# Kernel tuning notes

Measured on AMD Instinct MI355X. Metric: run time of the kernel, lower is better.

The kernel has to match this reference:

```python
import jax, jax.numpy as jnp
import numpy as np

D_MODEL = 1024
NHEAD = 16
DFF = 4096
EPS = 1e-5


def layer_norm(x, g, b, eps=EPS):
    mu = jnp.mean(x, axis=-1, keepdims=True)
    var = jnp.var(x, axis=-1, keepdims=True)
    return (x - mu) * jax.lax.rsqrt(var + eps) * g + b


def setup_inputs() -> dict:
    key = jax.random.key(0)
    ks = jax.random.split(key, 8)
    S, N, E = 1024, 8, D_MODEL
    s = 0.02
    return {
        "src": jax.random.normal(ks[0], (S, N, E), dtype=jnp.float32),
        "in_proj_w": jax.random.normal(ks[1], (3 * E, E), dtype=jnp.float32) * s,
        "in_proj_b": jnp.zeros((3 * E,), dtype=jnp.float32),
        "out_w": jax.random.normal(ks[2], (E, E), dtype=jnp.float32) * s,
        "out_b": jnp.zeros((E,), dtype=jnp.float32),
        "w1": jax.random.normal(ks[3], (DFF, E), dtype=jnp.float32) * s,
        "b1": jnp.zeros((DFF,), dtype=jnp.float32),
        "w2": jax.random.normal(ks[4], (E, DFF), dtype=jnp.float32) * s,
        "b2": jnp.zeros((E,), dtype=jnp.float32),
        "ln1_g": jnp.ones((E,), dtype=jnp.float32),
        "ln1_b": jnp.zeros((E,), dtype=jnp.float32),
        "ln2_g": jnp.ones((E,), dtype=jnp.float32),
        "ln2_b": jnp.zeros((E,), dtype=jnp.float32),
    }


def reference(src, in_proj_w, in_proj_b, out_w, out_b, w1, b1, w2, b2,
              ln1_g, ln1_b, ln2_g, ln2_b):
    S, N, E = src.shape
    H = NHEAD
    D = E // H
    scale = 1.0 / jnp.sqrt(jnp.asarray(D, src.dtype))

    # fused QKV projection (PyTorch in_proj): [S,N,3E]
    qkv = src @ in_proj_w.T + in_proj_b
    q, k, v = jnp.split(qkv, 3, axis=-1)
    # [S,N,E] -> [N,H,S,D]
    def to_heads(t):
        return t.reshape(S, N, H, D).transpose(1, 2, 0, 3)
    q, k, v = to_heads(q), to_heads(k), to_heads(v)

    # explicit QK^T / softmax / AV (need_weights=True path)
    scores = jnp.einsum('nhsd,nhtd->nhst', q * scale, k)  # [N,H,S,S]
    attn = jax.nn.softmax(scores, axis=-1)
    ctx = jnp.einsum('nhst,nhtd->nhsd', attn, v)          # [N,H,S,D]
    ctx = ctx.transpose(2, 0, 1, 3).reshape(S, N, E)
    attn_out = ctx @ out_w.T + out_b

    # avg over heads (PyTorch default average_attn_weights=True): [N,S,S]
    attn_weights = jnp.mean(attn, axis=1)

    # post-norm residual structure (norm_first=False), dropout=0 (eval)
    x = layer_norm(src + attn_out, ln1_g, ln1_b)
    ff = jax.nn.relu(x @ w1.T + b1) @ w2.T + b2
    x = layer_norm(x + ff, ln2_g, ln2_b)
    return x, attn_weights
```

## Files before the change

### kernel.cpp

```cpp
#include <hip/hip_runtime.h>

typedef __attribute__((ext_vector_type(4))) float f32x4;
typedef __attribute__((ext_vector_type(8))) short short8;
typedef __attribute__((ext_vector_type(4))) unsigned short u16x4;

#define MFMA(a,b,c) __builtin_amdgcn_mfma_f32_16x16x32_bf16(a,b,c,0,0,0)

__device__ __forceinline__ unsigned short f2bf(float x){
    union { float f; unsigned int u; } c; c.f = x;
    unsigned int u = c.u;
    unsigned int r = (u + 0x7fffu + ((u >> 16) & 1u)) >> 16;
    return (unsigned short)r;
}
__device__ __forceinline__ float bf2f(unsigned short h){
    union { unsigned int u; float f; } c; c.u = ((unsigned int)h) << 16;
    return c.f;
}

__device__ __forceinline__ void load16_lds(const unsigned short* g, unsigned short* l){
    __builtin_amdgcn_global_load_lds(
        (const __attribute__((address_space(1))) unsigned int*)g,
        (__attribute__((address_space(3))) unsigned int*)l, 16, 0, 0);
}

#define SWZ_IDX(row, col, stride) \
    ((row)*(stride) + (((((col) >> 3) ^ ((row) & 7)) << 3) | ((col) & 7)))

__global__ __launch_bounds__(256) void cast_f32_bf16(const float* __restrict__ in,
                                                     unsigned short* __restrict__ out, int n4){
    int i = blockIdx.x * 256 + threadIdx.x;
    if (i < n4){
        const float4* in4 = (const float4*)in;
        float4 v = in4[i];
        u16x4 o;
        o[0] = f2bf(v.x); o[1] = f2bf(v.y); o[2] = f2bf(v.z); o[3] = f2bf(v.w);
        ((u16x4*)out)[i] = o;
    }
}

template<int OUT_BF16, int RELU>
__global__ __launch_bounds__(512) void gemm256(const unsigned short* __restrict__ A,
                                               const unsigned short* __restrict__ W,
                                               const float* __restrict__ bias,
                                               void* __restrict__ Cout,
                                               int M, int N, int K)
{
    __shared__ unsigned short Asw[2][256*64];
    __shared__ unsigned short Bsw[2][256*64];
    const int tid  = threadIdx.x;
    const int wave = tid >> 6, lane = tid & 63;
    const int wr = wave >> 2, wc = wave & 3;
    const int lr = lane & 15, lg = lane >> 4;
    const int bm = blockIdx.x, bn = blockIdx.y;

    f32x4 acc[8][4] = {};

    const unsigned short* Ab = A + (size_t)bm*256*K;
    const unsigned short* Wb = W + (size_t)bn*256*K;

    auto stage = [&](int buf, int k0){
        #pragma unroll
        for (int i = 0; i < 4; ++i){
            int c = i*512 + tid;
            int row = c >> 3, sl = (c & 7) ^ (row & 7);
            load16_lds(Ab + (size_t)row*K + k0 + sl*8, &Asw[buf][0] + (size_t)c*8);
        }
        #pragma unroll
        for (int i = 0; i < 4; ++i){
            int c = i*512 + tid;
            int row = c >> 3, sl = (c & 7) ^ (row & 7);
            load16_lds(Wb + (size_t)row*K + k0 + sl*8, &Bsw[buf][0] + (size_t)c*8);
        }
    };

    stage(0, 0);
    const int NT = K >> 6;
    for (int t = 0; t < NT; ++t){
        const int cur = t & 1;
        if (t + 1 < NT){
            stage(cur ^ 1, (t+1) << 6);
            asm volatile("s_waitcnt vmcnt(8)" ::: "memory");
        } else {
            asm volatile("s_waitcnt vmcnt(0)" ::: "memory");
        }
        __builtin_amdgcn_s_barrier();
        asm volatile("" ::: "memory");
        const unsigned short* Al = &Asw[cur][0];
        const unsigned short* Bl = &Bsw[cur][0];
        #pragma unroll
        for (int kk = 0; kk < 2; ++kk){
            short8 af[8], bf[4];
            #pragma unroll
            for (int mi = 0; mi < 8; ++mi)
                af[mi] = *(const short8*)(Al + SWZ_IDX(wr*128 + mi*16 + lr, kk*32 + lg*8, 64));
            #pragma unroll
            for (int ni = 0; ni < 4; ++ni)
                bf[ni] = *(const short8*)(Bl + SWZ_IDX(wc*64 + ni*16 + lr, kk*32 + lg*8, 64));
            __builtin_amdgcn_s_setprio(1);
            #pragma unroll
            for (int mi = 0; mi < 8; ++mi)
                #pragma unroll
                for (int ni = 0; ni < 4; ++ni)
                    acc[mi][ni] = MFMA(af[mi], bf[ni], acc[mi][ni]);
            __builtin_amdgcn_s_setprio(0);
        }
        asm volatile("" ::: "memory");
        __builtin_amdgcn_s_barrier();
    }

    #pragma unroll
    for (int ni = 0; ni < 4; ++ni){
        int col = bn*256 + wc*64 + ni*16 + lr;
        float bv = bias ? bias[col] : 0.0f;
        #pragma unroll
        for (int mi = 0; mi < 8; ++mi){
            int row0 = bm*256 + wr*128 + mi*16 + lg*4;
            #pragma unroll
            for (int j = 0; j < 4; ++j){
                float v = acc[mi][ni][j] + bv;
                if (RELU) v = v > 0.0f ? v : 0.0f;
                if (OUT_BF16) ((unsigned short*)Cout)[(size_t)(row0+j)*N + col] = f2bf(v);
                else          ((float*)Cout)[(size_t)(row0+j)*N + col] = v;
            }
        }
    }
}

template<int OUT_BF16, int RELU>
__global__ __launch_bounds__(512) void gemm256x128(const unsigned short* __restrict__ A,
                                                   const unsigned short* __restrict__ W,
                                                   const float* __restrict__ bias,
                                                   void* __restrict__ Cout,
                                                   int M, int N, int K)
{
    __shared__ unsigned short Asw[2][256*64];
    __shared__ unsigned short Bsw[2][128*64];
    const int tid  = threadIdx.x;
    const int wave = tid >> 6, lane = tid & 63;
    const int wr = wave >> 1, wc = wave & 1;
    const int lr = lane & 15, lg = lane >> 4;
    const int bm = blockIdx.x, bn = blockIdx.y;

    f32x4 acc[4][4] = {};

    const unsigned short* Ab = A + (size_t)bm*256*K;
    const unsigned short* Wb = W + (size_t)bn*128*K;

    auto stage = [&](int buf, int k0){
        #pragma unroll
        for (int i = 0; i < 4; ++i){
            int c = i*512 + tid;
            int row = c >> 3, sl = (c & 7) ^ (row & 7);
            load16_lds(Ab + (size_t)row*K + k0 + sl*8, &Asw[buf][0] + (size_t)c*8);
        }
        #pragma unroll
        for (int i = 0; i < 2; ++i){
            int c = i*512 + tid;
            int row = c >> 3, sl = (c & 7) ^ (row & 7);
            load16_lds(Wb + (size_t)row*K + k0 + sl*8, &Bsw[buf][0] + (size_t)c*8);
        }
    };

    stage(0, 0);
    const int NT = K >> 6;
    for (int t = 0; t < NT; ++t){
        const int cur = t & 1;
        if (t + 1 < NT){
            stage(cur ^ 1, (t+1) << 6);
            asm volatile("s_waitcnt vmcnt(6)" ::: "memory");
        } else {
            asm volatile("s_waitcnt vmcnt(0)" ::: "memory");
        }
        __builtin_amdgcn_s_barrier();
        asm volatile("" ::: "memory");
        const unsigned short* Al = &Asw[cur][0];
        const unsigned short* Bl = &Bsw[cur][0];
        #pragma unroll
        for (int kk = 0; kk < 2; ++kk){
            short8 af[4], bf[4];
            #pragma unroll
            for (int mi = 0; mi < 4; ++mi)
                af[mi] = *(const short8*)(Al + SWZ_IDX(wr*64 + mi*16 + lr, kk*32 + lg*8, 64));
            #pragma unroll
            for (int ni = 0; ni < 4; ++ni)
                bf[ni] = *(const short8*)(Bl + SWZ_IDX(wc*64 + ni*16 + lr, kk*32 + lg*8, 64));
            __builtin_amdgcn_s_setprio(1);
            #pragma unroll
            for (int mi = 0; mi < 4; ++mi)
                #pragma unroll
                for (int ni = 0; ni < 4; ++ni)
                    acc[mi][ni] = MFMA(af[mi], bf[ni], acc[mi][ni]);
            __builtin_amdgcn_s_setprio(0);
        }
        asm volatile("" ::: "memory");
        __builtin_amdgcn_s_barrier();
    }

    #pragma unroll
    for (int ni = 0; ni < 4; ++ni){
        int col = bn*128 + wc*64 + ni*16 + lr;
        float bv = bias ? bias[col] : 0.0f;
        #pragma unroll
        for (int mi = 0; mi < 4; ++mi){
            int row0 = bm*256 + wr*64 + mi*16 + lg*4;
            #pragma unroll
            for (int j = 0; j < 4; ++j){
                float v = acc[mi][ni][j] + bv;
                if (RELU) v = v > 0.0f ? v : 0.0f;
                if (OUT_BF16) ((unsigned short*)Cout)[(size_t)(row0+j)*N + col] = f2bf(v);
                else          ((float*)Cout)[(size_t)(row0+j)*N + col] = v;
            }
        }
    }
}

__global__ __launch_bounds__(256) void transpose_v(const unsigned short* __restrict__ qkv,
                                                   unsigned short* __restrict__ vt)
{
    __shared__ unsigned short tile[64][80];
    const int tt = blockIdx.x, h = blockIdx.y, n = blockIdx.z;
    const int tid = threadIdx.x;
    #pragma unroll
    for (int i = 0; i < 2; ++i){
        int c = i*256 + tid;
        int row = c >> 3, cc = c & 7;
        short8 v = *(const short8*)(qkv + ((size_t)(tt*64+row)*8 + n)*3072 + 2048 + h*64 + cc*8);
        *(short8*)&tile[row][cc*8] = v;
    }
    __syncthreads();
    #pragma unroll
    for (int i = 0; i < 2; ++i){
        int c = i*256 + tid;
        int drow = c >> 3, cc = c & 7;
        short8 o;
        #pragma unroll
        for (int j = 0; j < 8; ++j) o[j] = tile[cc*8+j][drow];
        *(short8*)(vt + ((size_t)(n*16+h)*64 + drow)*1024 + tt*64 + cc*8) = o;
    }
}

__global__ __launch_bounds__(256) void attn_fused(const unsigned short* __restrict__ qkv,
                                                  const unsigned short* __restrict__ vt,
                                                  float2* __restrict__ stats,
                                                  unsigned short* __restrict__ ctx)
{
    __shared__ unsigned short qs[32*64];
    __shared__ unsigned short kt[64*64];
    __shared__ unsigned short vtile[64*64];
    __shared__ unsigned short pt[32*64];
    __shared__ float wl[4][32];
    __shared__ float rowinv[32];
    const int qb = blockIdx.x, h = blockIdx.y, n = blockIdx.z;
    const int tid = threadIdx.x;
    const int wave = tid >> 6, lane = tid & 63;
    const int lr = lane & 15, lg = lane >> 4;
    const int s0 = qb * 32;
    const float scale = 0.125f;

    {
        int row = tid >> 3, cc = tid & 7;
        *(short8*)(qs + SWZ_IDX(row, cc*8, 64)) =
            *(const short8*)(qkv + ((size_t)(s0+row)*8 + n)*3072 + h*64 + cc*8);
    }

    float lsum[2][4] = {};
    f32x4 av[2] = {};

    for (int tt = 0; tt < 16; ++tt){
        __syncthreads();
        #pragma unroll
        for (int i = 0; i < 2; ++i){
            int c = i*256 + wave*64 + lane;
            int row = c >> 3, sl = (c & 7) ^ (row & 7);
            load16_lds(qkv + ((size_t)(tt*64+row)*8 + n)*3072 + 1024 + h*64 + sl*8,
                       kt + (size_t)(i*256 + wave*64)*8);
            load16_lds(vt + ((size_t)(n*16+h)*64 + row)*1024 + tt*64 + sl*8,
                       vtile + (size_t)(i*256 + wave*64)*8);
        }
        __syncthreads();

        f32x4 acc[2] = {};
        #pragma unroll
        for (int kk = 0; kk < 2; ++kk){
            short8 b  = *(const short8*)(kt + SWZ_IDX(wave*16 + lr, kk*32 + lg*8, 64));
            short8 a0 = *(const short8*)(qs + SWZ_IDX(lr,          kk*32 + lg*8, 64));
            short8 a1 = *(const short8*)(qs + SWZ_IDX(16 + lr,     kk*32 + lg*8, 64));
            acc[0] = MFMA(a0, b, acc[0]);
            acc[1] = MFMA(a1, b, acc[1]);
        }
        #pragma unroll
        for (int mi = 0; mi < 2; ++mi)
            #pragma unroll
            for (int j = 0; j < 4; ++j){
                float p = __expf(fminf(acc[mi][j] * scale, 80.0f));
                lsum[mi][j] += p;
                pt[SWZ_IDX(mi*16 + lg*4 + j, wave*16 + lr, 64)] = f2bf(p);
            }
        __syncthreads();

        #pragma unroll
        for (int kk = 0; kk < 2; ++kk){
            short8 b  = *(const short8*)(vtile + SWZ_IDX(wave*16 + lr, kk*32 + lg*8, 64));
            short8 a0 = *(const short8*)(pt + SWZ_IDX(lr,      kk*32 + lg*8, 64));
            short8 a1 = *(const short8*)(pt + SWZ_IDX(16 + lr, kk*32 + lg*8, 64));
            av[0] = MFMA(a0, b, av[0]);
            av[1] = MFMA(a1, b, av[1]);
        }
    }

    #pragma unroll
    for (int mi = 0; mi < 2; ++mi)
        #pragma unroll
        for (int j = 0; j < 4; ++j){
            float v = lsum[mi][j];
            v += __shfl_xor(v, 1);
            v += __shfl_xor(v, 2);
            v += __shfl_xor(v, 4);
            v += __shfl_xor(v, 8);
            if (lr == 0) wl[wave][mi*16 + lg*4 + j] = v;
        }
    __syncthreads();
    if (tid < 32){
        float l = wl[0][tid] + wl[1][tid] + wl[2][tid] + wl[3][tid];
        float inv = 1.0f / l;
        rowinv[tid] = inv;
        stats[((size_t)(n*16+h)*1024) + s0 + tid] = make_float2(0.0f, inv * 0.0625f);
    }
    __syncthreads();

    #pragma unroll
    for (int mi = 0; mi < 2; ++mi)
        #pragma unroll
        for (int j = 0; j < 4; ++j){
            int lrow = mi*16 + lg*4 + j;
            int srow = s0 + lrow;
            int d = wave*16 + lr;
            ctx[((size_t)srow*8 + n)*1024 + h*64 + d] = f2bf(av[mi][j] * rowinv[lrow]);
        }
}

__global__ __launch_bounds__(256) void attn_mean(const unsigned short* __restrict__ qkv,
                                                 const float2* __restrict__ stats,
                                                 float* __restrict__ attw)
{
    __shared__ unsigned short qs[16*1024];
    __shared__ unsigned short kv[2][4][16*128];
    __shared__ float2 smL[16][16];
    const int qb = blockIdx.x, n = blockIdx.y;
    const int tid = threadIdx.x;
    const int wave = tid >> 6, lane = tid & 63;
    const int lr = lane & 15, lg = lane >> 4;
    const int s0 = qb * 16;
    const float scale = 0.125f;

    {
        int head = tid >> 4, row = tid & 15;
        smL[head][row] = stats[((size_t)(n*16+head)*1024) + s0 + row];
    }
    #pragma unroll
    for (int i = 0; i < 8; ++i){
        int c = i*256 + tid;
        int row = c >> 7, cc = c & 127;
        *(short8*)(qs + SWZ_IDX(row, cc*8, 1024)) =
            *(const short8*)(qkv + ((size_t)(s0+row)*8 + n)*3072 + cc*8);
    }

    unsigned short* kvw = &kv[0][wave][0];
    const int KVBUF = 4*16*128;

    auto stage = [&](int buf, int tt, int g){
        #pragma unroll
        for (int i = 0; i < 4; ++i){
            int c2 = i*64 + lane;
            int rw = c2 >> 4;
            int sd = c2 & 15;
            int sl = sd ^ (rw & 7);
            int trow = tt*64 + wave*16 + rw;
            load16_lds(qkv + ((size_t)trow*8 + n)*3072 + 1024 + g*128 + sl*8,
                       kvw + buf*KVBUF + i*512);
        }
    };

    __syncthreads();
    stage(0, 0, 0);

    float* obase = attw + (size_t)n*1024*1024;
    int r = 0;
    for (int tt = 0; tt < 16; ++tt){
        f32x4 racc = {0.0f, 0.0f, 0.0f, 0.0f};
        for (int g = 0; g < 8; ++g, ++r){
            int nr = r + 1;
            if (nr < 128) stage(nr & 1, nr >> 3, nr & 7);
            if (r < 127) asm volatile("s_waitcnt vmcnt(4)" ::: "memory");
            else         asm volatile("s_waitcnt vmcnt(0)" ::: "memory");
            const unsigned short* kb = kvw + (r & 1)*KVBUF;
            #pragma unroll
            for (int hh = 0; hh < 2; ++hh){
                f32x4 acc = {0.0f, 0.0f, 0.0f, 0.0f};
                #pragma unroll
                for (int kk = 0; kk < 2; ++kk){
                    short8 b = *(const short8*)(kb + SWZ_IDX(lr, hh*64 + kk*32 + lg*8, 128));
                    short8 a = *(const short8*)(qs + SWZ_IDX(lr, g*128 + hh*64 + kk*32 + lg*8, 1024));
                    acc = MFMA(a, b, acc);
                }
                #pragma unroll
                for (int j = 0; j < 4; ++j){
                    float2 mc = smL[g*2 + hh][lg*4 + j];
                    racc[j] += __expf(fminf(acc[j]*scale, 80.0f) - mc.x) * mc.y;
                }
            }
        }
        #pragma unroll
        for (int j = 0; j < 4; ++j)
            obase[(size_t)(s0 + lg*4 + j)*1024 + tt*64 + wave*16 + lr] = racc[j];
    }
}

__global__ __launch_bounds__(256) void add_ln(const float* __restrict__ a,
                                              const float* __restrict__ b,
                                              const float* __restrict__ g,
                                              const float* __restrict__ be,
                                              float* __restrict__ out32,
                                              unsigned short* __restrict__ outbf)
{
    __shared__ float red[8];
    const int row = blockIdx.x;
    const int tid = threadIdx.x;
    const int wave = tid >> 6, lane = tid & 63;
    float4 va = ((const float4*)(a + (size_t)row*1024))[tid];
    float4 vb = ((const float4*)(b + (size_t)row*1024))[tid];
    float x0 = va.x + vb.x, x1 = va.y + vb.y, x2 = va.z + vb.z, x3 = va.w + vb.w;
    float s  = x0 + x1 + x2 + x3;
    float sq = x0*x0 + x1*x1 + x2*x2 + x3*x3;
    #pragma unroll
    for (int off = 1; off < 64; off <<= 1){
        s  += __shfl_xor(s,  off);
        sq += __shfl_xor(sq, off);
    }
    if (lane == 0){ red[wave] = s; red[4+wave] = sq; }
    __syncthreads();
    s  = red[0] + red[1] + red[2] + red[3];
    sq = red[4] + red[5] + red[6] + red[7];
    float mean = s * (1.0f/1024.0f);
    float var  = sq * (1.0f/1024.0f) - mean*mean;
    float rstd = rsqrtf(var + 1e-5f);
    int c = tid * 4;
    float4 vg = ((const float4*)(g  + c))[0];
    float4 vbeta = ((const float4*)(be + c))[0];
    float y0 = (x0-mean)*rstd*vg.x + vbeta.x;
    float y1 = (x1-mean)*rstd*vg.y + vbeta.y;
    float y2 = (x2-mean)*rstd*vg.z + vbeta.z;
    float y3 = (x3-mean)*rstd*vg.w + vbeta.w;
    float4 o; o.x=y0; o.y=y1; o.z=y2; o.w=y3;
    ((float4*)(out32 + (size_t)row*1024))[tid] = o;
    if (outbf){
        u16x4 ob; ob[0]=f2bf(y0); ob[1]=f2bf(y1); ob[2]=f2bf(y2); ob[3]=f2bf(y3);
        ((u16x4*)(outbf + (size_t)row*1024))[tid] = ob;
    }
}

extern "C" void kernel_launch(void* const* d_in, const int* in_sizes, int n_in,
                              void* d_out, int out_size, void* d_ws, size_t ws_size,
                              hipStream_t stream)
{
    (void)in_sizes; (void)n_in; (void)out_size; (void)ws_size;
    const float* src  = (const float*)d_in[0];
    const float* wqkv = (const float*)d_in[1];
    const float* bqkv = (const float*)d_in[2];
    const float* wout = (const float*)d_in[3];
    const float* bout = (const float*)d_in[4];
    const float* w1   = (const float*)d_in[5];
    const float* b1   = (const float*)d_in[6];
    const float* w2   = (const float*)d_in[7];
    const float* b2   = (const float*)d_in[8];
    const float* g1   = (const float*)d_in[9];
    const float* be1  = (const float*)d_in[10];
    const float* g2   = (const float*)d_in[11];
    const float* be2  = (const float*)d_in[12];

    char* ws = (char*)d_ws;
    const size_t MB = 1ull << 20;
    unsigned short* wqkv_bf = (unsigned short*)(ws + 0*MB);
    unsigned short* wout_bf = (unsigned short*)(ws + 6*MB);
    unsigned short* w1_bf   = (unsigned short*)(ws + 8*MB);
    unsigned short* w2_bf   = (unsigned short*)(ws + 16*MB);
    unsigned short* src_bf  = (unsigned short*)(ws + 24*MB);
    unsigned short* x1_bf   = (unsigned short*)(ws + 24*MB);
    unsigned short* qkv_bf  = (unsigned short*)(ws + 40*MB);
    unsigned short* vt_bf   = (unsigned short*)(ws + 88*MB);
    unsigned short* ff1_bf  = (unsigned short*)(ws + 40*MB);
    unsigned short* ctx_bf  = (unsigned short*)(ws + 104*MB);
    float* attn_out = (float*)(ws + 120*MB);
    float* ff2_f32  = (float*)(ws + 120*MB);
    float* x1_f32   = (float*)(ws + 152*MB);
    float2* stats   = (float2*)(ws + 184*MB);

    float* x_out    = (float*)d_out;
    float* attw_out = (float*)d_out + (size_t)8192*1024;

    auto cast = [&](const float* in, unsigned short* out, int nelem){
        int n4 = nelem / 4;
        hipLaunchKernelGGL(cast_f32_bf16, dim3((n4 + 255)/256), dim3(256), 0, stream, in, out, n4);
    };
    cast(wqkv, wqkv_bf, 3072*1024);
    cast(wout, wout_bf, 1024*1024);
    cast(w1,   w1_bf,   4096*1024);
    cast(w2,   w2_bf,   1024*4096);
    cast(src,  src_bf,  8192*1024);

    hipLaunchKernelGGL((gemm256<1,0>), dim3(32,12), dim3(512), 0, stream,
                       src_bf, wqkv_bf, bqkv, (void*)qkv_bf, 8192, 3072, 1024);
    hipLaunchKernelGGL(transpose_v, dim3(16,16,8), dim3(256), 0, stream, qkv_bf, vt_bf);
    hipLaunchKernelGGL(attn_fused, dim3(32,16,8), dim3(256), 0, stream,
                       qkv_bf, vt_bf, stats, ctx_bf);
    hipLaunchKernelGGL(attn_mean, dim3(64,8), dim3(256), 0, stream,
                       qkv_bf, stats, attw_out);
    hipLaunchKernelGGL((gemm256x128<0,0>), dim3(32,8), dim3(512), 0, stream,
                       ctx_bf, wout_bf, bout, (void*)attn_out, 8192, 1024, 1024);
    hipLaunchKernelGGL(add_ln, dim3(8192), dim3(256), 0, stream,
                       src, attn_out, g1, be1, x1_f32, x1_bf);
    hipLaunchKernelGGL((gemm256<1,1>), dim3(32,16), dim3(512), 0, stream,
                       x1_bf, w1_bf, b1, (void*)ff1_bf, 8192, 4096, 1024);
    hipLaunchKernelGGL((gemm256x128<0,0>), dim3(32,8), dim3(512), 0, stream,
                       ff1_bf, w2_bf, b2, (void*)ff2_f32, 8192, 1024, 4096);
    hipLaunchKernelGGL(add_ln, dim3(8192), dim3(256), 0, stream,
                       x1_f32, ff2_f32, g2, be2, x_out, nullptr);
}
```

Before: 545.5 us.

## Double-buffer K/V tiles in fused attention and shrink softmax stats to scalar

The attention kernel now prefetches the next K and V tiles into a second LDS buffer while it computes on the current ones. It waits with vmcnt counting instead of two full __syncthreads per tile, which relies on each wave only reading the rows it loaded itself. The P-tile write is moved between raw s_barriers. The per-row stats shrink from float2 to float, dropping a subtraction of a max term that was always zero in the mean-weights kernel. This removes exposed load latency and some barrier and exp work, at the cost of twice the LDS for K and V.

```diff
diff --git a/kernel.cpp b/kernel.cpp
--- a/kernel.cpp
+++ b/kernel.cpp
@@ -241,12 +241,12 @@
 
 __global__ __launch_bounds__(256) void attn_fused(const unsigned short* __restrict__ qkv,
                                                   const unsigned short* __restrict__ vt,
-                                                  float2* __restrict__ stats,
+                                                  float* __restrict__ stats,
                                                   unsigned short* __restrict__ ctx)
 {
     __shared__ unsigned short qs[32*64];
-    __shared__ unsigned short kt[64*64];
-    __shared__ unsigned short vtile[64*64];
+    __shared__ unsigned short kt[2][64*64];
+    __shared__ unsigned short vtile[2][64*64];
     __shared__ unsigned short pt[32*64];
     __shared__ float wl[4][32];
     __shared__ float rowinv[32];
@@ -263,44 +263,66 @@
             *(const short8*)(qkv + ((size_t)(s0+row)*8 + n)*3072 + h*64 + cc*8);
     }
 
+    auto stageKV = [&](int buf, int tt){
+        #pragma unroll
+        for (int i = 0; i < 2; ++i){
+            int c = wave*128 + i*64 + lane;
+            int row = c >> 3, sl = (c & 7) ^ (row & 7);
+            load16_lds(qkv + ((size_t)(tt*64+row)*8 + n)*3072 + 1024 + h*64 + sl*8,
+                       &kt[buf][0] + (size_t)c*8);
+            load16_lds(vt + ((size_t)(n*16+h)*64 + row)*1024 + tt*64 + sl*8,
+                       &vtile[buf][0] + (size_t)c*8);
+        }
+    };
+
+    stageKV(0, 0);
+    __syncthreads();
+
     float lsum[2][4] = {};
     f32x4 av[2] = {};
 
     for (int tt = 0; tt < 16; ++tt){
-        __syncthreads();
-        #pragma unroll
-        for (int i = 0; i < 2; ++i){
-            int c = i*256 + wave*64 + lane;
-            int row = c >> 3, sl = (c & 7) ^ (row & 7);
-            load16_lds(qkv + ((size_t)(tt*64+row)*8 + n)*3072 + 1024 + h*64 + sl*8,
-                       kt + (size_t)(i*256 + wave*64)*8);
-            load16_lds(vt + ((size_t)(n*16+h)*64 + row)*1024 + tt*64 + sl*8,
-                       vtile + (size_t)(i*256 + wave*64)*8);
-        }
-        __syncthreads();
+        const int cur = tt & 1;
+        if (tt + 1 < 16){
+            stageKV(cur ^ 1, tt + 1);
+            asm volatile("s_waitcnt vmcnt(4)" ::: "memory");
+        } else {
+            asm volatile("s_waitcnt vmcnt(0)" ::: "memory");
+        }
+        asm volatile("" ::: "memory");
 
         f32x4 acc[2] = {};
         #pragma unroll
         for (int kk = 0; kk < 2; ++kk){
-            short8 b  = *(const short8*)(kt + SWZ_IDX(wave*16 + lr, kk*32 + lg*8, 64));
-            short8 a0 = *(const short8*)(qs + SWZ_IDX(lr,          kk*32 + lg*8, 64));
-            short8 a1 = *(const short8*)(qs + SWZ_IDX(16 + lr,     kk*32 + lg*8, 64));
+            short8 b  = *(const short8*)(&kt[cur][0] + SWZ_IDX(wave*16 + lr, kk*32 + lg*8, 64));
+            short8 a0 = *(const short8*)(qs + SWZ_IDX(lr,      kk*32 + lg*8, 64));
+            short8 a1 = *(const short8*)(qs + SWZ_IDX(16 + lr, kk*32 + lg*8, 64));
             acc[0] = MFMA(a0, b, acc[0]);
             acc[1] = MFMA(a1, b, acc[1]);
         }
+        unsigned short pv16[2][4];
         #pragma unroll
         for (int mi = 0; mi < 2; ++mi)
             #pragma unroll
             for (int j = 0; j < 4; ++j){
                 float p = __expf(fminf(acc[mi][j] * scale, 80.0f));
                 lsum[mi][j] += p;
-                pt[SWZ_IDX(mi*16 + lg*4 + j, wave*16 + lr, 64)] = f2bf(p);
+                pv16[mi][j] = f2bf(p);
             }
-        __syncthreads();
+
+        __builtin_amdgcn_s_barrier();
+        asm volatile("" ::: "memory");
+        #pragma unroll
+        for (int mi = 0; mi < 2; ++mi)
+            #pragma unroll
+            for (int j = 0; j < 4; ++j)
+                pt[SWZ_IDX(mi*16 + lg*4 + j, wave*16 + lr, 64)] = pv16[mi][j];
+        asm volatile("" ::: "memory");
+        __builtin_amdgcn_s_barrier();
 
         #pragma unroll
         for (int kk = 0; kk < 2; ++kk){
-            short8 b  = *(const short8*)(vtile + SWZ_IDX(wave*16 + lr, kk*32 + lg*8, 64));
+            short8 b  = *(const short8*)(&vtile[cur][0] + SWZ_IDX(wave*16 + lr, kk*32 + lg*8, 64));
             short8 a0 = *(const short8*)(pt + SWZ_IDX(lr,      kk*32 + lg*8, 64));
             short8 a1 = *(const short8*)(pt + SWZ_IDX(16 + lr, kk*32 + lg*8, 64));
             av[0] = MFMA(a0, b, av[0]);
@@ -324,7 +346,7 @@
         float l = wl[0][tid] + wl[1][tid] + wl[2][tid] + wl[3][tid];
         float inv = 1.0f / l;
         rowinv[tid] = inv;
-        stats[((size_t)(n*16+h)*1024) + s0 + tid] = make_float2(0.0f, inv * 0.0625f);
+        stats[((size_t)(n*16+h)*1024) + s0 + tid] = inv * 0.0625f;
     }
     __syncthreads();
 
@@ -340,12 +362,12 @@
 }
 
 __global__ __launch_bounds__(256) void attn_mean(const unsigned short* __restrict__ qkv,
-                                                 const float2* __restrict__ stats,
+                                                 const float* __restrict__ stats,
                                                  float* __restrict__ attw)
 {
     __shared__ unsigned short qs[16*1024];
     __shared__ unsigned short kv[2][4][16*128];
-    __shared__ float2 smL[16][16];
+    __shared__ float smL[16][16];
     const int qb = blockIdx.x, n = blockIdx.y;
     const int tid = threadIdx.x;
     const int wave = tid >> 6, lane = tid & 63;
@@ -405,8 +427,8 @@
                 }
                 #pragma unroll
                 for (int j = 0; j < 4; ++j){
-                    float2 mc = smL[g*2 + hh][lg*4 + j];
-                    racc[j] += __expf(fminf(acc[j]*scale, 80.0f) - mc.x) * mc.y;
+                    float sm = smL[g*2 + hh][lg*4 + j];
+                    racc[j] += __expf(fminf(acc[j]*scale, 80.0f)) * sm;
                 }
             }
         }
@@ -493,7 +515,7 @@
     float* attn_out = (float*)(ws + 120*MB);
     float* ff2_f32  = (float*)(ws + 120*MB);
     float* x1_f32   = (float*)(ws + 152*MB);
-    float2* stats   = (float2*)(ws + 184*MB);
+    float* stats    = (float*)(ws + 184*MB);
 
     float* x_out    = (float*)d_out;
     float* attw_out = (float*)d_out + (size_t)8192*1024;
```

Measured after the change: 550.8 us. No clear change (+1.0%).
